# Performance work log

Hardware: AMD Instinct MI355X
Metric: run time of the kernel (lower is better)

The kernel has to match this reference:

```python
import jax, jax.numpy as jnp
import numpy as np

B = 256
N_SNP = 100000
BITS = 4          # snp_onehot_bits
BLOCK = 20        # SNPs per block
N_BLOCKS = N_SNP // BLOCK            # 5000 output blocks
IN_DIM = N_SNP * BITS                # 400000
DIMS = [1024, 256]
OUT_DIM = 1
LN_EPS = 1e-5


def _make_indices():
    # blocks_gt[i] = [20*i, ..., 20*i+19]; replicate get_param4sparse
    blocks = np.arange(N_SNP, dtype=np.int64).reshape(N_BLOCKS, BLOCK)
    idx0 = (blocks[:, :, None] * BITS + np.arange(BITS)).reshape(-1)   # input bit index, [nnz]
    idx1 = np.repeat(np.arange(N_BLOCKS, dtype=np.int64), BLOCK * BITS)  # output block index, [nnz]
    return jnp.asarray(idx0, jnp.int32), jnp.asarray(idx1, jnp.int32)


def setup_inputs() -> dict:
    key = jax.random.key(0)
    ks = jax.random.split(key, 9)
    idx0, idx1 = _make_indices()
    x = jax.random.uniform(ks[0], (B, IN_DIM), dtype=jnp.float32)
    sparse_values = jax.random.normal(ks[1], (idx0.shape[0],), dtype=jnp.float32)
    ln_gamma = jnp.ones((N_BLOCKS,), jnp.float32)
    ln_beta = jnp.zeros((N_BLOCKS,), jnp.float32)
    s1 = 1.0 / np.sqrt(N_BLOCKS)
    W1 = jax.random.uniform(ks[2], (DIMS[0], N_BLOCKS), jnp.float32, -s1, s1)
    b1 = jax.random.uniform(ks[3], (DIMS[0],), jnp.float32, -s1, s1)
    s2 = 1.0 / np.sqrt(DIMS[0])
    W2 = jax.random.uniform(ks[4], (DIMS[1], DIMS[0]), jnp.float32, -s2, s2)
    b2 = jax.random.uniform(ks[5], (DIMS[1],), jnp.float32, -s2, s2)
    s3 = 1.0 / np.sqrt(DIMS[1])
    W3 = jax.random.uniform(ks[6], (OUT_DIM, DIMS[1]), jnp.float32, -s3, s3)
    b3 = jax.random.uniform(ks[7], (OUT_DIM,), jnp.float32, -s3, s3)
    return {"x": x, "sparse_values": sparse_values, "ln_gamma": ln_gamma,
            "ln_beta": ln_beta, "W1": W1, "b1": b1, "W2": W2, "b2": b2,
            "W3": W3, "b3": b3, "idx0": idx0, "idx1": idx1}


def reference(x, sparse_values, ln_gamma, ln_beta, W1, b1, W2, b2, W3, b3, idx0, idx1):
    # SparseLinear: out[b, j] = sum_{k: idx1[k]==j} sparse_values[k] * x[b, idx0[k]]
    gathered = x[:, idx0] * sparse_values[None, :]                       # [B, nnz]
    gblocks = jax.ops.segment_sum(gathered.T, idx1, num_segments=N_BLOCKS).T  # [B, n_blocks]
    # LayerNorm over block dim
    mu = jnp.mean(gblocks, axis=-1, keepdims=True)
    var = jnp.mean(jnp.square(gblocks - mu), axis=-1, keepdims=True)
    h = (gblocks - mu) * jax.lax.rsqrt(var + LN_EPS) * ln_gamma + ln_beta
    # Dense head (note: no activation after first Linear, faithful to source)
    h = h @ W1.T + b1
    h = h @ W2.T + b2
    h = jax.nn.sigmoid(h)
    return h @ W3.T + b3                                                 # [B, OUT_DIM]
```

## Files before the change

### kernel.cpp

```cpp
#include <hip/hip_runtime.h>
#include <math.h>

#define BATCH   256
#define NBLK    5000
#define NBLKP   5024
#define IN_DIM  400000
#define D1      1024
#define D2      256
#define K1P     5120
#define NSPLIT  8
#define KSPLIT  (K1P / NSPLIT)

#define CONV_BLKS   (D1 + D2 * D1 / 1024)
#define SPARSE_BLKS ((NBLKP + 63) / 64 * BATCH)

typedef __attribute__((ext_vector_type(8))) short short8_t;
typedef __attribute__((ext_vector_type(4))) float f32x4;

static __device__ __forceinline__ unsigned short f2bf(float f) {
    union { float f; unsigned int u; } v; v.f = f;
    unsigned int u = v.u;
    return (unsigned short)((u + 0x7FFFu + ((u >> 16) & 1u)) >> 16);
}

__global__ __launch_bounds__(256) void k_stage1(const float* __restrict__ x,
                                                const float* __restrict__ sv,
                                                float* __restrict__ g,
                                                const float* __restrict__ W1,
                                                unsigned short* __restrict__ W1b,
                                                const float* __restrict__ W2,
                                                unsigned short* __restrict__ W2b) {
    const int id  = blockIdx.x;
    const int tid = threadIdx.x;
    if (id < CONV_BLKS) {
        if (id < D1) {
            const float* src = W1 + (size_t)id * NBLK;
            unsigned short* dst = W1b + (size_t)id * K1P;
            for (int c4 = tid; c4 < K1P / 4; c4 += 256) {
                const int c = c4 * 4;
                ushort4 o;
                if (c < NBLK) {
                    float4 v = *reinterpret_cast<const float4*>(src + c);
                    o = { f2bf(v.x), f2bf(v.y), f2bf(v.z), f2bf(v.w) };
                } else {
                    o = ushort4{0, 0, 0, 0};
                }
                *reinterpret_cast<ushort4*>(dst + c) = o;
            }
        } else {
            const int idx = ((id - D1) * 256 + tid) * 4;
            float4 v = *reinterpret_cast<const float4*>(W2 + idx);
            ushort4 o = { f2bf(v.x), f2bf(v.y), f2bf(v.z), f2bf(v.w) };
            *reinterpret_cast<ushort4*>(W2b + idx) = o;
        }
        return;
    }
    const int rem = id - CONV_BLKS;
    const int b   = rem / ((NBLKP + 63) / 64);
    const int bx  = rem % ((NBLKP + 63) / 64);
    const int jj  = tid >> 2;
    const int s   = tid & 3;
    const int j   = bx * 64 + jj;
    if (j >= NBLK) return;
    const float4* xr = reinterpret_cast<const float4*>(x + (size_t)b * IN_DIM + (size_t)j * 80);
    const float4* sr = reinterpret_cast<const float4*>(sv + (size_t)j * 80);
    float acc = 0.0f;
#pragma unroll
    for (int r = 0; r < 5; ++r) {
        float4 xv = xr[r * 4 + s];
        float4 sg = sr[r * 4 + s];
        acc += xv.x * sg.x + xv.y * sg.y + xv.z * sg.z + xv.w * sg.w;
    }
    acc += __shfl_xor(acc, 1);
    acc += __shfl_xor(acc, 2);
    if (s == 0) g[(size_t)b * NBLKP + j] = acc;
}

__global__ __launch_bounds__(256) void k_ln(const float* __restrict__ g,
                                            const float* __restrict__ gamma,
                                            const float* __restrict__ beta,
                                            unsigned short* __restrict__ A) {
    const int b   = blockIdx.x;
    const int tid = threadIdx.x;
    const float* row = g + (size_t)b * NBLKP;
    float v[20];
    float s = 0.0f, ss = 0.0f;
#pragma unroll
    for (int i = 0; i < 20; ++i) {
        const int j = tid + i * 256;
        const float xv = (j < NBLK) ? row[j] : 0.0f;
        v[i] = xv; s += xv; ss += xv * xv;
    }
#pragma unroll
    for (int o = 32; o > 0; o >>= 1) {
        s  += __shfl_xor(s, o);
        ss += __shfl_xor(ss, o);
    }
    __shared__ float ls[4], lss[4];
    const int wid = tid >> 6;
    if ((tid & 63) == 0) { ls[wid] = s; lss[wid] = ss; }
    __syncthreads();
    s  = ls[0] + ls[1] + ls[2] + ls[3];
    ss = lss[0] + lss[1] + lss[2] + lss[3];
    const float mu  = s / (float)NBLK;
    const float var = ss / (float)NBLK - mu * mu;
    const float rs  = rsqrtf(var + 1e-5f);
    unsigned short* dst = A + (size_t)b * K1P;
#pragma unroll
    for (int i = 0; i < 20; ++i) {
        const int j = tid + i * 256;
        const float val = (j < NBLK) ? ((v[i] - mu) * rs * gamma[j] + beta[j]) : 0.0f;
        dst[j] = f2bf(val);
    }
}

__global__ __launch_bounds__(256) void k_mfma_gemm1(const unsigned short* __restrict__ A,
                                                    const unsigned short* __restrict__ W,
                                                    float* __restrict__ C,
                                                    int ksteps) {
    const int m0 = blockIdx.y * 64;
    const int n0 = blockIdx.x * 64;
    const int z  = blockIdx.z;
    const int kbase = z * ksteps * 64;
    float* Cz = C + (size_t)z * (size_t)BATCH * D1;

    __shared__ unsigned short As[64][72];
    __shared__ unsigned short Ws[64][72];

    const int tid  = threadIdx.x;
    const int wave = tid >> 6;
    const int lane = tid & 63;
    const int wr   = (wave >> 1) * 32;
    const int wc   = (wave & 1) * 32;
    const int lr   = lane & 15;
    const int lk   = (lane >> 4) * 8;
    const int srow = tid >> 3;
    const int scol = (tid & 7) * 8;

    const unsigned short* Ap = A + (size_t)(m0 + srow) * K1P + kbase + scol;
    const unsigned short* Wp = W + (size_t)(n0 + srow) * K1P + kbase + scol;

    short8_t pa0 = *reinterpret_cast<const short8_t*>(Ap);
    short8_t pa1 = *reinterpret_cast<const short8_t*>(Ap + (size_t)32 * K1P);
    short8_t pw0 = *reinterpret_cast<const short8_t*>(Wp);
    short8_t pw1 = *reinterpret_cast<const short8_t*>(Wp + (size_t)32 * K1P);

    f32x4 acc[2][2] = {};

    for (int t = 0; t < ksteps; ++t) {
        __syncthreads();
        *reinterpret_cast<short8_t*>(&As[srow][scol])      = pa0;
        *reinterpret_cast<short8_t*>(&As[srow + 32][scol]) = pa1;
        *reinterpret_cast<short8_t*>(&Ws[srow][scol])      = pw0;
        *reinterpret_cast<short8_t*>(&Ws[srow + 32][scol]) = pw1;
        __syncthreads();
        if (t + 1 < ksteps) {
            const unsigned short* An = Ap + (size_t)(t + 1) * 64;
            const unsigned short* Wn = Wp + (size_t)(t + 1) * 64;
            pa0 = *reinterpret_cast<const short8_t*>(An);
            pa1 = *reinterpret_cast<const short8_t*>(An + (size_t)32 * K1P);
            pw0 = *reinterpret_cast<const short8_t*>(Wn);
            pw1 = *reinterpret_cast<const short8_t*>(Wn + (size_t)32 * K1P);
        }
#pragma unroll
        for (int kk = 0; kk < 64; kk += 32) {
            short8_t a0 = *reinterpret_cast<const short8_t*>(&As[wr + lr][kk + lk]);
            short8_t a1 = *reinterpret_cast<const short8_t*>(&As[wr + 16 + lr][kk + lk]);
            short8_t b0 = *reinterpret_cast<const short8_t*>(&Ws[wc + lr][kk + lk]);
            short8_t b1 = *reinterpret_cast<const short8_t*>(&Ws[wc + 16 + lr][kk + lk]);
            acc[0][0] = __builtin_amdgcn_mfma_f32_16x16x32_bf16(a0, b0, acc[0][0], 0, 0, 0);
            acc[0][1] = __builtin_amdgcn_mfma_f32_16x16x32_bf16(a0, b1, acc[0][1], 0, 0, 0);
            acc[1][0] = __builtin_amdgcn_mfma_f32_16x16x32_bf16(a1, b0, acc[1][0], 0, 0, 0);
            acc[1][1] = __builtin_amdgcn_mfma_f32_16x16x32_bf16(a1, b1, acc[1][1], 0, 0, 0);
        }
    }

    const int rbase = (lane >> 4) * 4;
#pragma unroll
    for (int i = 0; i < 2; ++i)
#pragma unroll
        for (int j = 0; j < 2; ++j) {
            const int col = n0 + wc + j * 16 + lr;
#pragma unroll
            for (int r = 0; r < 4; ++r) {
                const int row = m0 + wr + i * 16 + rbase + r;
                Cz[(size_t)row * D1 + col] = acc[i][j][r];
            }
        }
}

__global__ __launch_bounds__(256) void k_fuse(const float* __restrict__ p,
                                              const float* __restrict__ b1,
                                              unsigned short* __restrict__ A2) {
    const int idx = (blockIdx.x * 256 + threadIdx.x) * 4;
    const int col = idx & (D1 - 1);
    const size_t S = (size_t)BATCH * D1;
    float4 bb = *reinterpret_cast<const float4*>(b1 + col);
    float sx = bb.x, sy = bb.y, sz = bb.z, sw = bb.w;
#pragma unroll
    for (int q = 0; q < NSPLIT; ++q) {
        float4 v = *reinterpret_cast<const float4*>(p + q * S + idx);
        sx += v.x; sy += v.y; sz += v.z; sw += v.w;
    }
    ushort4 o = { f2bf(sx), f2bf(sy), f2bf(sz), f2bf(sw) };
    *reinterpret_cast<ushort4*>(A2 + idx) = o;
}

__global__ __launch_bounds__(256) void k_tail(const unsigned short* __restrict__ A2,
                                              const unsigned short* __restrict__ W2b,
                                              const float* __restrict__ b2,
                                              const float* __restrict__ W3,
                                              const float* __restrict__ b3,
                                              float* __restrict__ out) {
    const int m0 = blockIdx.x * 32;
    __shared__ unsigned short As[32][72];
    __shared__ unsigned short Ws[256][72];
    __shared__ float red[4][32];

    const int tid  = threadIdx.x;
    const int wave = tid >> 6;
    const int lane = tid & 63;
    const int wc   = wave * 64;
    const int lr   = lane & 15;
    const int lk   = (lane >> 4) * 8;
    const int srow = tid >> 3;
    const int scol = (tid & 7) * 8;

    const unsigned short* Ap = A2 + (size_t)(m0 + srow) * D1 + scol;
    const unsigned short* Wp = W2b + (size_t)srow * D1 + scol;

    short8_t pa = *reinterpret_cast<const short8_t*>(Ap);
    short8_t pw[8];
#pragma unroll
    for (int it = 0; it < 8; ++it)
        pw[it] = *reinterpret_cast<const short8_t*>(Wp + (size_t)it * 32 * D1);

    f32x4 acc[2][4] = {};

    for (int t = 0; t < 16; ++t) {
        __syncthreads();
        *reinterpret_cast<short8_t*>(&As[srow][scol]) = pa;
#pragma unroll
        for (int it = 0; it < 8; ++it)
            *reinterpret_cast<short8_t*>(&Ws[srow + it * 32][scol]) = pw[it];
        __syncthreads();
        if (t + 1 < 16) {
            const int ko = (t + 1) * 64;
            pa = *reinterpret_cast<const short8_t*>(Ap + ko);
#pragma unroll
            for (int it = 0; it < 8; ++it)
                pw[it] = *reinterpret_cast<const short8_t*>(Wp + (size_t)it * 32 * D1 + ko);
        }
#pragma unroll
        for (int kk = 0; kk < 64; kk += 32) {
            short8_t a0 = *reinterpret_cast<const short8_t*>(&As[lr][kk + lk]);
            short8_t a1 = *reinterpret_cast<const short8_t*>(&As[16 + lr][kk + lk]);
#pragma unroll
            for (int j = 0; j < 4; ++j) {
                short8_t bj = *reinterpret_cast<const short8_t*>(&Ws[wc + j * 16 + lr][kk + lk]);
                acc[0][j] = __builtin_amdgcn_mfma_f32_16x16x32_bf16(a0, bj, acc[0][j], 0, 0, 0);
                acc[1][j] = __builtin_amdgcn_mfma_f32_16x16x32_bf16(a1, bj, acc[1][j], 0, 0, 0);
            }
        }
    }

    float b2c[4], w3c[4];
#pragma unroll
    for (int j = 0; j < 4; ++j) {
        const int col = wc + j * 16 + lr;
        b2c[j] = b2[col];
        w3c[j] = W3[col];
    }
    const int rbase = (lane >> 4) * 4;
#pragma unroll
    for (int i = 0; i < 2; ++i) {
#pragma unroll
        for (int r = 0; r < 4; ++r) {
            float pv = 0.0f;
#pragma unroll
            for (int j = 0; j < 4; ++j) {
                const float h = acc[i][j][r] + b2c[j];
                pv += w3c[j] / (1.0f + __expf(-h));
            }
            pv += __shfl_xor(pv, 1);
            pv += __shfl_xor(pv, 2);
            pv += __shfl_xor(pv, 4);
            pv += __shfl_xor(pv, 8);
            if (lr == 0) red[wave][i * 16 + rbase + r] = pv;
        }
    }
    __syncthreads();
    if (tid < 32) {
        const float s = red[0][tid] + red[1][tid] + red[2][tid] + red[3][tid];
        out[m0 + tid] = s + b3[0];
    }
}

extern "C" void kernel_launch(void* const* d_in, const int* in_sizes, int n_in,
                              void* d_out, int out_size, void* d_ws, size_t ws_size,
                              hipStream_t stream) {
    const float* x     = (const float*)d_in[0];
    const float* sv    = (const float*)d_in[1];
    const float* gamma = (const float*)d_in[2];
    const float* beta  = (const float*)d_in[3];
    const float* W1    = (const float*)d_in[4];
    const float* b1    = (const float*)d_in[5];
    const float* W2    = (const float*)d_in[6];
    const float* b2    = (const float*)d_in[7];
    const float* W3    = (const float*)d_in[8];
    const float* b3    = (const float*)d_in[9];
    float* out = (float*)d_out;

    char* ws = (char*)d_ws;
    size_t off = 0;
    auto alloc = [&](size_t bytes) { char* p = ws + off; off = (off + bytes + 255) & ~(size_t)255; return p; };
    float*          g     = (float*)         alloc((size_t)BATCH * NBLKP * 4);
    unsigned short* Ab    = (unsigned short*)alloc((size_t)BATCH * K1P * 2);
    unsigned short* W1b   = (unsigned short*)alloc((size_t)D1 * K1P * 2);
    float*          out1p = (float*)         alloc((size_t)NSPLIT * BATCH * D1 * 4);
    unsigned short* A2b   = (unsigned short*)alloc((size_t)BATCH * D1 * 2);
    unsigned short* W2b   = (unsigned short*)alloc((size_t)D2 * D1 * 2);

    k_stage1<<<dim3(CONV_BLKS + SPARSE_BLKS), 256, 0, stream>>>(x, sv, g, W1, W1b, W2, W2b);
    k_ln<<<dim3(BATCH), 256, 0, stream>>>(g, gamma, beta, Ab);
    k_mfma_gemm1<<<dim3(D1 / 64, BATCH / 64, NSPLIT), 256, 0, stream>>>(Ab, W1b, out1p, KSPLIT / 64);
    k_fuse<<<dim3(BATCH * D1 / (256 * 4)), 256, 0, stream>>>(out1p, b1, A2b);
    k_tail<<<dim3(BATCH / 32), 256, 0, stream>>>(A2b, W2b, b2, W3, b3, out);
}
```

Measured before the change: 136.9 us.

## Convert W1 to bf16 inside GEMM1, widen M tile, move W2 conversion to fuse

Drops the separate pass that converts W1 to bf16 in stage1. GEMM1 now loads fp32 W1 directly and converts it while staging into shared memory, which saves writing and re-reading a 10 MB bf16 copy. GEMM1 now covers all 256 batch rows per block with a 4x4 MFMA tile per wave and uses a split-K of 16. The W2 conversion moves into k_fuse, and k_tail goes to 512 threads with half the columns per wave, adding occupancy and partial-sum traffic in exchange.

```diff
diff --git a/kernel.cpp b/kernel.cpp
--- a/kernel.cpp
+++ b/kernel.cpp
@@ -8,11 +8,9 @@
 #define D1      1024
 #define D2      256
 #define K1P     5120
-#define NSPLIT  8
-#define KSPLIT  (K1P / NSPLIT)
-
-#define CONV_BLKS   (D1 + D2 * D1 / 1024)
-#define SPARSE_BLKS ((NBLKP + 63) / 64 * BATCH)
+#define NSPLIT  16
+#define ZK      (K1P / NSPLIT)
+#define ZSTEPS  (ZK / 64)
 
 typedef __attribute__((ext_vector_type(8))) short short8_t;
 typedef __attribute__((ext_vector_type(4))) float f32x4;
@@ -23,44 +21,14 @@
     return (unsigned short)((u + 0x7FFFu + ((u >> 16) & 1u)) >> 16);
 }
 
-__global__ __launch_bounds__(256) void k_stage1(const float* __restrict__ x,
+__global__ __launch_bounds__(256) void k_sparse(const float* __restrict__ x,
                                                 const float* __restrict__ sv,
-                                                float* __restrict__ g,
-                                                const float* __restrict__ W1,
-                                                unsigned short* __restrict__ W1b,
-                                                const float* __restrict__ W2,
-                                                unsigned short* __restrict__ W2b) {
-    const int id  = blockIdx.x;
+                                                float* __restrict__ g) {
+    const int b   = blockIdx.y;
     const int tid = threadIdx.x;
-    if (id < CONV_BLKS) {
-        if (id < D1) {
-            const float* src = W1 + (size_t)id * NBLK;
-            unsigned short* dst = W1b + (size_t)id * K1P;
-            for (int c4 = tid; c4 < K1P / 4; c4 += 256) {
-                const int c = c4 * 4;
-                ushort4 o;
-                if (c < NBLK) {
-                    float4 v = *reinterpret_cast<const float4*>(src + c);
-                    o = { f2bf(v.x), f2bf(v.y), f2bf(v.z), f2bf(v.w) };
-                } else {
-                    o = ushort4{0, 0, 0, 0};
-                }
-                *reinterpret_cast<ushort4*>(dst + c) = o;
-            }
-        } else {
-            const int idx = ((id - D1) * 256 + tid) * 4;
-            float4 v = *reinterpret_cast<const float4*>(W2 + idx);
-            ushort4 o = { f2bf(v.x), f2bf(v.y), f2bf(v.z), f2bf(v.w) };
-            *reinterpret_cast<ushort4*>(W2b + idx) = o;
-        }
-        return;
-    }
-    const int rem = id - CONV_BLKS;
-    const int b   = rem / ((NBLKP + 63) / 64);
-    const int bx  = rem % ((NBLKP + 63) / 64);
     const int jj  = tid >> 2;
     const int s   = tid & 3;
-    const int j   = bx * 64 + jj;
+    const int j   = blockIdx.x * 64 + jj;
     if (j >= NBLK) return;
     const float4* xr = reinterpret_cast<const float4*>(x + (size_t)b * IN_DIM + (size_t)j * 80);
     const float4* sr = reinterpret_cast<const float4*>(sv + (size_t)j * 80);
@@ -114,76 +82,93 @@
     }
 }
 
-__global__ __launch_bounds__(256) void k_mfma_gemm1(const unsigned short* __restrict__ A,
-                                                    const unsigned short* __restrict__ W,
-                                                    float* __restrict__ C,
-                                                    int ksteps) {
-    const int m0 = blockIdx.y * 64;
+__global__ __launch_bounds__(256) void k_gemm1(const unsigned short* __restrict__ A,
+                                               const float* __restrict__ W1,
+                                               float* __restrict__ C) {
     const int n0 = blockIdx.x * 64;
-    const int z  = blockIdx.z;
-    const int kbase = z * ksteps * 64;
-    float* Cz = C + (size_t)z * (size_t)BATCH * D1;
-
-    __shared__ unsigned short As[64][72];
+    const int z  = blockIdx.y;
+    const int kbase = z * ZK;
+    float* Cz = C + (size_t)z * BATCH * D1;
+
+    __shared__ unsigned short As[256][72];
     __shared__ unsigned short Ws[64][72];
 
     const int tid  = threadIdx.x;
     const int wave = tid >> 6;
     const int lane = tid & 63;
-    const int wr   = (wave >> 1) * 32;
-    const int wc   = (wave & 1) * 32;
     const int lr   = lane & 15;
     const int lk   = (lane >> 4) * 8;
     const int srow = tid >> 3;
     const int scol = (tid & 7) * 8;
-
-    const unsigned short* Ap = A + (size_t)(m0 + srow) * K1P + kbase + scol;
-    const unsigned short* Wp = W + (size_t)(n0 + srow) * K1P + kbase + scol;
-
-    short8_t pa0 = *reinterpret_cast<const short8_t*>(Ap);
-    short8_t pa1 = *reinterpret_cast<const short8_t*>(Ap + (size_t)32 * K1P);
-    short8_t pw0 = *reinterpret_cast<const short8_t*>(Wp);
-    short8_t pw1 = *reinterpret_cast<const short8_t*>(Wp + (size_t)32 * K1P);
-
-    f32x4 acc[2][2] = {};
-
-    for (int t = 0; t < ksteps; ++t) {
+    const int wrow = tid >> 2;
+    const int wcol = (tid & 3) * 16;
+
+    const unsigned short* Ap = A + (size_t)srow * K1P + kbase + scol;
+    const float* Wrow = W1 + (size_t)(n0 + wrow) * NBLK;
+
+    short8_t pa[8];
+    float4 pwf[4];
+    auto loadA = [&](int t) {
+#pragma unroll
+        for (int it = 0; it < 8; ++it)
+            pa[it] = *reinterpret_cast<const short8_t*>(Ap + (size_t)it * 32 * K1P + t * 64);
+    };
+    auto loadW = [&](int t) {
+        const int k0 = kbase + t * 64 + wcol;
+#pragma unroll
+        for (int q = 0; q < 4; ++q) {
+            const int k = k0 + q * 4;
+            pwf[q] = (k < NBLK) ? *reinterpret_cast<const float4*>(Wrow + k)
+                                : float4{0.f, 0.f, 0.f, 0.f};
+        }
+    };
+
+    loadA(0);
+    loadW(0);
+
+    f32x4 acc[4][4] = {};
+
+    for (int t = 0; t < ZSTEPS; ++t) {
         __syncthreads();
-        *reinterpret_cast<short8_t*>(&As[srow][scol])      = pa0;
-        *reinterpret_cast<short8_t*>(&As[srow + 32][scol]) = pa1;
-        *reinterpret_cast<short8_t*>(&Ws[srow][scol])      = pw0;
-        *reinterpret_cast<short8_t*>(&Ws[srow + 32][scol]) = pw1;
+#pragma unroll
+        for (int it = 0; it < 8; ++it)
+            *reinterpret_cast<short8_t*>(&As[srow + it * 32][scol]) = pa[it];
+        {
+            short8_t w0 = { (short)f2bf(pwf[0].x), (short)f2bf(pwf[0].y), (short)f2bf(pwf[0].z), (short)f2bf(pwf[0].w),
+                            (short)f2bf(pwf[1].x), (short)f2bf(pwf[1].y), (short)f2bf(pwf[1].z), (short)f2bf(pwf[1].w) };
+            short8_t w1 = { (short)f2bf(pwf[2].x), (short)f2bf(pwf[2].y), (short)f2bf(pwf[2].z), (short)f2bf(pwf[2].w),
+                            (short)f2bf(pwf[3].x), (short)f2bf(pwf[3].y), (short)f2bf(pwf[3].z), (short)f2bf(pwf[3].w) };
+            *reinterpret_cast<short8_t*>(&Ws[wrow][wcol])     = w0;
+            *reinterpret_cast<short8_t*>(&Ws[wrow][wcol + 8]) = w1;
+        }
         __syncthreads();
-        if (t + 1 < ksteps) {
-            const unsigned short* An = Ap + (size_t)(t + 1) * 64;
-            const unsigned short* Wn = Wp + (size_t)(t + 1) * 64;
-            pa0 = *reinterpret_cast<const short8_t*>(An);
-            pa1 = *reinterpret_cast<const short8_t*>(An + (size_t)32 * K1P);
-            pw0 = *reinterpret_cast<const short8_t*>(Wn);
-            pw1 = *reinterpret_cast<const short8_t*>(Wn + (size_t)32 * K1P);
-        }
+        if (t + 1 < ZSTEPS) { loadA(t + 1); loadW(t + 1); }
 #pragma unroll
         for (int kk = 0; kk < 64; kk += 32) {
-            short8_t a0 = *reinterpret_cast<const short8_t*>(&As[wr + lr][kk + lk]);
-            short8_t a1 = *reinterpret_cast<const short8_t*>(&As[wr + 16 + lr][kk + lk]);
-            short8_t b0 = *reinterpret_cast<const short8_t*>(&Ws[wc + lr][kk + lk]);
-            short8_t b1 = *reinterpret_cast<const short8_t*>(&Ws[wc + 16 + lr][kk + lk]);
-            acc[0][0] = __builtin_amdgcn_mfma_f32_16x16x32_bf16(a0, b0, acc[0][0], 0, 0, 0);
-            acc[0][1] = __builtin_amdgcn_mfma_f32_16x16x32_bf16(a0, b1, acc[0][1], 0, 0, 0);
-            acc[1][0] = __builtin_amdgcn_mfma_f32_16x16x32_bf16(a1, b0, acc[1][0], 0, 0, 0);
-            acc[1][1] = __builtin_amdgcn_mfma_f32_16x16x32_bf16(a1, b1, acc[1][1], 0, 0, 0);
+            short8_t a[4], b[4];
+#pragma unroll
+            for (int i = 0; i < 4; ++i)
+                a[i] = *reinterpret_cast<const short8_t*>(&As[wave * 64 + i * 16 + lr][kk + lk]);
+#pragma unroll
+            for (int j = 0; j < 4; ++j)
+                b[j] = *reinterpret_cast<const short8_t*>(&Ws[j * 16 + lr][kk + lk]);
+#pragma unroll
+            for (int i = 0; i < 4; ++i)
+#pragma unroll
+                for (int j = 0; j < 4; ++j)
+                    acc[i][j] = __builtin_amdgcn_mfma_f32_16x16x32_bf16(a[i], b[j], acc[i][j], 0, 0, 0);
         }
     }
 
     const int rbase = (lane >> 4) * 4;
 #pragma unroll
-    for (int i = 0; i < 2; ++i)
-#pragma unroll
-        for (int j = 0; j < 2; ++j) {
-            const int col = n0 + wc + j * 16 + lr;
+    for (int i = 0; i < 4; ++i)
+#pragma unroll
+        for (int j = 0; j < 4; ++j) {
+            const int col = n0 + j * 16 + lr;
 #pragma unroll
             for (int r = 0; r < 4; ++r) {
-                const int row = m0 + wr + i * 16 + rbase + r;
+                const int row = wave * 64 + i * 16 + rbase + r;
                 Cz[(size_t)row * D1 + col] = acc[i][j][r];
             }
         }
@@ -191,7 +176,9 @@
 
 __global__ __launch_bounds__(256) void k_fuse(const float* __restrict__ p,
                                               const float* __restrict__ b1,
-                                              unsigned short* __restrict__ A2) {
+                                              unsigned short* __restrict__ A2,
+                                              const float* __restrict__ W2,
+                                              unsigned short* __restrict__ W2b) {
     const int idx = (blockIdx.x * 256 + threadIdx.x) * 4;
     const int col = idx & (D1 - 1);
     const size_t S = (size_t)BATCH * D1;
@@ -204,9 +191,12 @@
     }
     ushort4 o = { f2bf(sx), f2bf(sy), f2bf(sz), f2bf(sw) };
     *reinterpret_cast<ushort4*>(A2 + idx) = o;
-}
-
-__global__ __launch_bounds__(256) void k_tail(const unsigned short* __restrict__ A2,
+    float4 wv = *reinterpret_cast<const float4*>(W2 + idx);
+    ushort4 wo = { f2bf(wv.x), f2bf(wv.y), f2bf(wv.z), f2bf(wv.w) };
+    *reinterpret_cast<ushort4*>(W2b + idx) = wo;
+}
+
+__global__ __launch_bounds__(512) void k_tail(const unsigned short* __restrict__ A2,
                                               const unsigned short* __restrict__ W2b,
                                               const float* __restrict__ b2,
                                               const float* __restrict__ W3,
@@ -215,12 +205,12 @@
     const int m0 = blockIdx.x * 32;
     __shared__ unsigned short As[32][72];
     __shared__ unsigned short Ws[256][72];
-    __shared__ float red[4][32];
+    __shared__ float red[8][32];
 
     const int tid  = threadIdx.x;
     const int wave = tid >> 6;
     const int lane = tid & 63;
-    const int wc   = wave * 64;
+    const int wc   = wave * 32;
     const int lr   = lane & 15;
     const int lk   = (lane >> 4) * 8;
     const int srow = tid >> 3;
@@ -229,34 +219,35 @@
     const unsigned short* Ap = A2 + (size_t)(m0 + srow) * D1 + scol;
     const unsigned short* Wp = W2b + (size_t)srow * D1 + scol;
 
-    short8_t pa = *reinterpret_cast<const short8_t*>(Ap);
-    short8_t pw[8];
-#pragma unroll
-    for (int it = 0; it < 8; ++it)
-        pw[it] = *reinterpret_cast<const short8_t*>(Wp + (size_t)it * 32 * D1);
-
-    f32x4 acc[2][4] = {};
+    short8_t pa = {};
+    short8_t pw[4];
+    if (tid < 256) pa = *reinterpret_cast<const short8_t*>(Ap);
+#pragma unroll
+    for (int it = 0; it < 4; ++it)
+        pw[it] = *reinterpret_cast<const short8_t*>(Wp + (size_t)it * 64 * D1);
+
+    f32x4 acc[2][2] = {};
 
     for (int t = 0; t < 16; ++t) {
         __syncthreads();
-        *reinterpret_cast<short8_t*>(&As[srow][scol]) = pa;
-#pragma unroll
-        for (int it = 0; it < 8; ++it)
-            *reinterpret_cast<short8_t*>(&Ws[srow + it * 32][scol]) = pw[it];
+        if (tid < 256) *reinterpret_cast<short8_t*>(&As[srow][scol]) = pa;
+#pragma unroll
+        for (int it = 0; it < 4; ++it)
+            *reinterpret_cast<short8_t*>(&Ws[srow + it * 64][scol]) = pw[it];
         __syncthreads();
         if (t + 1 < 16) {
             const int ko = (t + 1) * 64;
-            pa = *reinterpret_cast<const short8_t*>(Ap + ko);
-#pragma unroll
-            for (int it = 0; it < 8; ++it)
-                pw[it] = *reinterpret_cast<const short8_t*>(Wp + (size_t)it * 32 * D1 + ko);
+            if (tid < 256) pa = *reinterpret_cast<const short8_t*>(Ap + ko);
+#pragma unroll
+            for (int it = 0; it < 4; ++it)
+                pw[it] = *reinterpret_cast<const short8_t*>(Wp + (size_t)it * 64 * D1 + ko);
         }
 #pragma unroll
         for (int kk = 0; kk < 64; kk += 32) {
             short8_t a0 = *reinterpret_cast<const short8_t*>(&As[lr][kk + lk]);
             short8_t a1 = *reinterpret_cast<const short8_t*>(&As[16 + lr][kk + lk]);
 #pragma unroll
-            for (int j = 0; j < 4; ++j) {
+            for (int j = 0; j < 2; ++j) {
                 short8_t bj = *reinterpret_cast<const short8_t*>(&Ws[wc + j * 16 + lr][kk + lk]);
                 acc[0][j] = __builtin_amdgcn_mfma_f32_16x16x32_bf16(a0, bj, acc[0][j], 0, 0, 0);
                 acc[1][j] = __builtin_amdgcn_mfma_f32_16x16x32_bf16(a1, bj, acc[1][j], 0, 0, 0);
@@ -264,9 +255,9 @@
         }
     }
 
-    float b2c[4], w3c[4];
-#pragma unroll
-    for (int j = 0; j < 4; ++j) {
+    float b2c[2], w3c[2];
+#pragma unroll
+    for (int j = 0; j < 2; ++j) {
         const int col = wc + j * 16 + lr;
         b2c[j] = b2[col];
         w3c[j] = W3[col];
@@ -278,7 +269,7 @@
         for (int r = 0; r < 4; ++r) {
             float pv = 0.0f;
 #pragma unroll
-            for (int j = 0; j < 4; ++j) {
+            for (int j = 0; j < 2; ++j) {
                 const float h = acc[i][j][r] + b2c[j];
                 pv += w3c[j] / (1.0f + __expf(-h));
             }
@@ -291,8 +282,10 @@
     }
     __syncthreads();
     if (tid < 32) {
-        const float s = red[0][tid] + red[1][tid] + red[2][tid] + red[3][tid];
-        out[m0 + tid] = s + b3[0];
+        float s2 = 0.0f;
+#pragma unroll
+        for (int w = 0; w < 8; ++w) s2 += red[w][tid];
+        out[m0 + tid] = s2 + b3[0];
     }
 }
 
@@ -316,14 +309,13 @@
     auto alloc = [&](size_t bytes) { char* p = ws + off; off = (off + bytes + 255) & ~(size_t)255; return p; };
     float*          g     = (float*)         alloc((size_t)BATCH * NBLKP * 4);
     unsigned short* Ab    = (unsigned short*)alloc((size_t)BATCH * K1P * 2);
-    unsigned short* W1b   = (unsigned short*)alloc((size_t)D1 * K1P * 2);
     float*          out1p = (float*)         alloc((size_t)NSPLIT * BATCH * D1 * 4);
     unsigned short* A2b   = (unsigned short*)alloc((size_t)BATCH * D1 * 2);
     unsigned short* W2b   = (unsigned short*)alloc((size_t)D2 * D1 * 2);
 
-    k_stage1<<<dim3(CONV_BLKS + SPARSE_BLKS), 256, 0, stream>>>(x, sv, g, W1, W1b, W2, W2b);
+    k_sparse<<<dim3((NBLK + 63) / 64, BATCH), 256, 0, stream>>>(x, sv, g);
     k_ln<<<dim3(BATCH), 256, 0, stream>>>(g, gamma, beta, Ab);
-    k_mfma_gemm1<<<dim3(D1 / 64, BATCH / 64, NSPLIT), 256, 0, stream>>>(Ab, W1b, out1p, KSPLIT / 64);
-    k_fuse<<<dim3(BATCH * D1 / (256 * 4)), 256, 0, stream>>>(out1p, b1, A2b);
-    k_tail<<<dim3(BATCH / 32), 256, 0, stream>>>(A2b, W2b, b2, W3, b3, out);
-}
+    k_gemm1<<<dim3(D1 / 64, NSPLIT), 256, 0, stream>>>(Ab, W1, out1p);
+    k_fuse<<<dim3(BATCH * D1 / (256 * 4)), 256, 0, stream>>>(out1p, b1, A2b, W2, W2b);
+    k_tail<<<dim3(BATCH / 32), 512, 0, stream>>>(A2b, W2b, b2, W3, b3, out);
+}
```

Result: faster. 128.8 us (-5.9%).
